# Kernel tuning notes

Measured on AMD Instinct MI355X. Metric: run time of the kernel, lower is better.

## Reference

```python
import jax, jax.numpy as jnp
import numpy as np

N = 100000
E = 1200000
D_IN = 64
D_OUT = 64
NUM_TYPES = 2


def setup_inputs() -> dict:
    key = jax.random.key(0)
    k1, k2, k3, k4, k5 = jax.random.split(key, 5)
    x = jax.random.normal(k1, (N, D_IN), dtype=jnp.float32)
    W = jax.random.normal(k2, (NUM_TYPES, D_IN, D_OUT), dtype=jnp.float32) / np.sqrt(D_IN)
    b = jax.random.normal(k3, (NUM_TYPES, D_OUT), dtype=jnp.float32) * 0.01
    edge_index = jax.random.randint(k4, (2, E), 0, N, dtype=jnp.int64)
    edge_attr = jax.random.randint(k5, (E,), 0, NUM_TYPES, dtype=jnp.int64)
    return {"x": x, "W": W, "b": b, "edge_index": edge_index, "edge_attr": edge_attr}


def reference(x, W, b, edge_index, edge_attr):
    # PyG flow source_to_target: x_j = x[src], aggregate at dst
    src, dst = edge_index[0], edge_index[1]
    x_j = x[src]                                   # [E, D_IN] gather
    # HeteroLinear with 2 types: compute both small GEMMs, select per edge
    m0 = x_j @ W[0] + b[0]                          # [E, D_OUT]
    m1 = x_j @ W[1] + b[1]                          # [E, D_OUT]
    msg = jnp.where((edge_attr == 0)[:, None], m0, m1)
    # scatter-max aggregation; PyG fills nodes with no incoming edges with 0
    agg = jax.ops.segment_max(msg, dst, num_segments=x.shape[0])
    out = jnp.where(jnp.isneginf(agg), 0.0, agg)
    return out
```

## Files before the change

kernel.cpp:

```cpp
#include <hip/hip_runtime.h>
#include <math.h>

static constexpr int D = 64;
static constexpr int SCAN_BLOCKS = 256;
static constexpr int NB_CHUNK = 96;
static constexpr int BIN_SHIFT = 6;
static constexpr int MAXBINS = 2048;

typedef __bf16 bf16x8 __attribute__((ext_vector_type(8)));
typedef float f32x4 __attribute__((ext_vector_type(4)));


__device__ __forceinline__ unsigned short f2bf(float f) {
  unsigned u = __float_as_uint(f);
  return (unsigned short)((u + 0x7fffu + ((u >> 16) & 1u)) >> 16);
}
__device__ __forceinline__ float bf2f(unsigned short h) {
  return __uint_as_float((unsigned)h << 16);
}

__device__ __forceinline__ void lds_max_f32(float* p, float v) {
  if (v >= 0.0f)
    atomicMax(reinterpret_cast<int*>(p), __float_as_int(v));
  else
    atomicMin(reinterpret_cast<unsigned int*>(p), __float_as_uint(v));
}

__device__ __forceinline__ void atomic_max_float(float* p, float v, float cur) {
  if (!(v > cur)) return;
  if (v >= 0.0f)
    atomicMax(reinterpret_cast<int*>(p), __float_as_int(v));
  else
    atomicMin(reinterpret_cast<unsigned int*>(p), __float_as_uint(v));
}

__global__ void k_init_neginf(float4* __restrict__ out, int n4) {
  int i = blockIdx.x * blockDim.x + threadIdx.x;
  if (i < n4) {
    float4 v;
    v.x = v.y = v.z = v.w = -INFINITY;
    out[i] = v;
  }
}

__global__ __launch_bounds__(256) void k_gemm(
    const float* __restrict__ x, const float* __restrict__ W,
    const float* __restrict__ b, unsigned short* __restrict__ yb, int nN) {
  const int lane = threadIdx.x & 63;
  const int wid = (blockIdx.x << 2) + (threadIdx.x >> 6);
  const int nWaves = gridDim.x << 2;
  const int kgrp = (lane >> 4) << 3;
  const int nsub = lane & 15;

  bf16x8 Bf[8][2];
  float bias[8];
#pragma unroll
  for (int nt = 0; nt < 8; ++nt) {
    const int t = nt >> 2;
    const int n = ((nt & 3) << 4) + nsub;
#pragma unroll
    for (int ks = 0; ks < 2; ++ks) {
      bf16x8 f;
#pragma unroll
      for (int e = 0; e < 8; ++e) {
        const int k = (ks << 5) + kgrp + e;
        f[e] = (__bf16)W[t * 4096 + k * 64 + n];
      }
      Bf[nt][ks] = f;
    }
    bias[nt] = b[t * 64 + n];
  }

  const int nChunks = (nN + 15) >> 4;
  for (int c = wid; c < nChunks; c += nWaves) {
    const int base = c << 4;
    const int arow = min(base + nsub, nN - 1);
    const float4 xa0 = *reinterpret_cast<const float4*>(x + (size_t)arow * 64 + kgrp);
    const float4 xa1 = *reinterpret_cast<const float4*>(x + (size_t)arow * 64 + kgrp + 4);
    const float4 xb0 = *reinterpret_cast<const float4*>(x + (size_t)arow * 64 + 32 + kgrp);
    const float4 xb1 = *reinterpret_cast<const float4*>(x + (size_t)arow * 64 + 36 + kgrp);
    bf16x8 a0, a1;
    a0[0] = (__bf16)xa0.x; a0[1] = (__bf16)xa0.y; a0[2] = (__bf16)xa0.z; a0[3] = (__bf16)xa0.w;
    a0[4] = (__bf16)xa1.x; a0[5] = (__bf16)xa1.y; a0[6] = (__bf16)xa1.z; a0[7] = (__bf16)xa1.w;
    a1[0] = (__bf16)xb0.x; a1[1] = (__bf16)xb0.y; a1[2] = (__bf16)xb0.z; a1[3] = (__bf16)xb0.w;
    a1[4] = (__bf16)xb1.x; a1[5] = (__bf16)xb1.y; a1[6] = (__bf16)xb1.z; a1[7] = (__bf16)xb1.w;
#pragma unroll
    for (int nt = 0; nt < 8; ++nt) {
      f32x4 acc = {bias[nt], bias[nt], bias[nt], bias[nt]};
      acc = __builtin_amdgcn_mfma_f32_16x16x32_bf16(a0, Bf[nt][0], acc, 0, 0, 0);
      acc = __builtin_amdgcn_mfma_f32_16x16x32_bf16(a1, Bf[nt][1], acc, 0, 0, 0);
      const int t = nt >> 2;
      const int o = ((nt & 3) << 4) + nsub;
      const int rbase = base + ((lane >> 4) << 2);
#pragma unroll
      for (int r = 0; r < 4; ++r) {
        const int node = rbase + r;
        if (node < nN) yb[((size_t)t * nN + node) * 64 + o] = f2bf(acc[r]);
      }
    }
  }
}


__global__ __launch_bounds__(1024) void k_lochist(const int* __restrict__ dst,
                                                  int* __restrict__ countsT,
                                                  int nE, int nBins, int chunk) {
  __shared__ int lh[MAXBINS];
  const int t = threadIdx.x;
  for (int i = t; i < nBins; i += 1024) lh[i] = 0;
  __syncthreads();
  const int beg = blockIdx.x * chunk;
  const int end = min(beg + chunk, nE);
  for (int i = beg + t; i < end; i += 1024) atomicAdd(&lh[dst[i] >> BIN_SHIFT], 1);
  __syncthreads();
  for (int i = t; i < nBins; i += 1024)
    countsT[(size_t)i * gridDim.x + blockIdx.x] = lh[i];
}

__global__ __launch_bounds__(256) void k_scan_partial(
    const int* __restrict__ counts, int* __restrict__ blockSums, int nN) {
  __shared__ int red[256];
  const int t = threadIdx.x;
  const int seg = (nN + gridDim.x - 1) / gridDim.x;
  const int beg = blockIdx.x * seg;
  const int end = min(beg + seg, nN);
  int s = 0;
  for (int i = beg + t; i < end; i += 256) s += counts[i];
  red[t] = s;
  __syncthreads();
  for (int d = 128; d > 0; d >>= 1) {
    if (t < d) red[t] += red[t + d];
    __syncthreads();
  }
  if (t == 0) blockSums[blockIdx.x] = red[0];
}

__global__ __launch_bounds__(256) void k_scan_block(
    int* __restrict__ blockSums, int* __restrict__ offs, int nN, int nBlocks) {
  __shared__ int sh[256];
  const int t = threadIdx.x;
  const int v = (t < nBlocks) ? blockSums[t] : 0;
  sh[t] = v;
  __syncthreads();
  for (int d = 1; d < 256; d <<= 1) {
    const int o = (t >= d) ? sh[t - d] : 0;
    __syncthreads();
    sh[t] += o;
    __syncthreads();
  }
  if (t < nBlocks) blockSums[t] = sh[t] - v;
  if (t == 255) offs[nN] = sh[255];
}

__global__ __launch_bounds__(256) void k_scan_write(
    const int* __restrict__ counts, const int* __restrict__ blockSums,
    int* __restrict__ offs, int nN) {
  __shared__ int sh[256];
  const int t = threadIdx.x;
  const int seg = (nN + gridDim.x - 1) / gridDim.x;
  const int beg = blockIdx.x * seg;
  const int end = min(beg + seg, nN);
  int carry = blockSums[blockIdx.x];
  for (int base = beg; base < end; base += 256) {
    const int i = base + t;
    const int v = (i < end) ? counts[i] : 0;
    sh[t] = v;
    __syncthreads();
    for (int d = 1; d < 256; d <<= 1) {
      const int o = (t >= d) ? sh[t - d] : 0;
      __syncthreads();
      sh[t] += o;
      __syncthreads();
    }
    if (i < end) offs[i] = carry + sh[t] - v;
    carry += sh[255];
    __syncthreads();
  }
}

__global__ __launch_bounds__(1024) void k_cscatter(
    const int* __restrict__ src, const int* __restrict__ dst,
    const int* __restrict__ ea, const int* __restrict__ offs,
    unsigned* __restrict__ rec, int nE, int nBins, int chunk) {
  __shared__ int cur[MAXBINS];
  const int t = threadIdx.x;
  for (int i = t; i < nBins; i += 1024)
    cur[i] = offs[(size_t)i * gridDim.x + blockIdx.x];
  __syncthreads();
  const int beg = blockIdx.x * chunk;
  const int end = min(beg + chunk, nE);
  for (int i = beg + t; i < end; i += 1024) {
    const int d = dst[i];
    const int pos = atomicAdd(&cur[d >> BIN_SHIFT], 1);
    rec[pos] = (unsigned)src[i] | ((unsigned)ea[i] << 20) |
               ((unsigned)(d & ((1 << BIN_SHIFT) - 1)) << 21);
  }
}

__global__ __launch_bounds__(256) void k_reduce_bin(
    const int* __restrict__ offs, const unsigned* __restrict__ rec,
    const unsigned short* __restrict__ yb, float* __restrict__ out, int nN) {
  __shared__ float acc[64 * 64];
  const int t = threadIdx.x;
#pragma unroll
  for (int i = 0; i < 16; ++i) acc[t + i * 256] = -INFINITY;
  __syncthreads();

  const int bin = blockIdx.x;
  const int beg = offs[bin * NB_CHUNK];
  const int cnt = offs[(bin + 1) * NB_CHUNK] - beg;
  const int w = t >> 6;
  const unsigned lane = t & 63;
  const unsigned nNu = (unsigned)nN;
  const int myBeg = beg + ((cnt * w) >> 2);
  const int myEnd = beg + ((cnt * (w + 1)) >> 2);

  int j = myBeg;
  for (; j + 7 < myEnd; j += 8) {
    unsigned r[8];
    float v[8];
#pragma unroll
    for (int q = 0; q < 8; ++q) r[q] = rec[j + q];
#pragma unroll
    for (int q = 0; q < 8; ++q)
      v[q] = bf2f(yb[((((r[q] >> 20) & 1u) * nNu + (r[q] & 0xFFFFFu)) << 6) + lane]);
#pragma unroll
    for (int q = 0; q < 8; ++q)
      lds_max_f32(&acc[(((r[q] >> 21) & 63u) << 6) + lane], v[q]);
  }
  for (; j + 3 < myEnd; j += 4) {
    unsigned r[4];
    float v[4];
#pragma unroll
    for (int q = 0; q < 4; ++q) r[q] = rec[j + q];
#pragma unroll
    for (int q = 0; q < 4; ++q)
      v[q] = bf2f(yb[((((r[q] >> 20) & 1u) * nNu + (r[q] & 0xFFFFFu)) << 6) + lane]);
#pragma unroll
    for (int q = 0; q < 4; ++q)
      lds_max_f32(&acc[(((r[q] >> 21) & 63u) << 6) + lane], v[q]);
  }
  for (; j < myEnd; ++j) {
    const unsigned r0 = rec[j];
    const float v0 = bf2f(yb[((((r0 >> 20) & 1u) * nNu + (r0 & 0xFFFFFu)) << 6) + lane]);
    lds_max_f32(&acc[(((r0 >> 21) & 63u) << 6) + lane], v0);
  }
  __syncthreads();

  const int nodeBase = bin << 6;
  for (int f = t; f < 64 * 16; f += 256) {
    const int node = nodeBase + (f >> 4);
    if (node < nN) {
      float4 v = *reinterpret_cast<const float4*>(&acc[f * 4]);
      if (v.x == -INFINITY) v.x = 0.0f;
      if (v.y == -INFINITY) v.y = 0.0f;
      if (v.z == -INFINITY) v.z = 0.0f;
      if (v.w == -INFINITY) v.w = 0.0f;
      *reinterpret_cast<float4*>(&out[(size_t)node * 64 + (f & 15) * 4]) = v;
    }
  }
}


__global__ void k_fixup(float4* __restrict__ out, int n4) {
  int i = blockIdx.x * blockDim.x + threadIdx.x;
  if (i < n4) {
    float4 v = out[i];
    if (v.x == -INFINITY) v.x = 0.0f;
    if (v.y == -INFINITY) v.y = 0.0f;
    if (v.z == -INFINITY) v.z = 0.0f;
    if (v.w == -INFINITY) v.w = 0.0f;
    out[i] = v;
  }
}

__global__ __launch_bounds__(256) void k_edge_direct(
    const float* __restrict__ x, const float* __restrict__ W,
    const float* __restrict__ b, const int* __restrict__ ei,
    const int* __restrict__ ea, float* __restrict__ out, int nEdges) {
  __shared__ float Wl[2 * D * D];
  __shared__ float bl[2 * D];
  for (int i = threadIdx.x; i < 2 * D * D; i += 256) Wl[i] = W[i];
  for (int i = threadIdx.x; i < 2 * D; i += 256) bl[i] = b[i];
  __syncthreads();
  const int wave = threadIdx.x >> 6;
  const int lane = threadIdx.x & 63;
  for (int e = blockIdx.x * 4 + wave; e < nEdges; e += gridDim.x * 4) {
    const int src = ei[e];
    const int dst = ei[nEdges + e];
    const int t = ea[e];
    const float xk = x[(size_t)src * D + lane];
    float acc = bl[t * D + lane];
    const float* Wt = &Wl[t * D * D];
#pragma unroll
    for (int k = 0; k < D; ++k)
      acc = fmaf(__shfl(xk, k, 64), Wt[k * D + lane], acc);
    float* p = out + (size_t)dst * D + lane;
    const float cur = *p;
    atomic_max_float(p, acc, cur);
  }
}


extern "C" void kernel_launch(void* const* d_in, const int* in_sizes, int n_in,
                              void* d_out, int out_size, void* d_ws, size_t ws_size,
                              hipStream_t stream) {
  const float* x = (const float*)d_in[0];
  const float* W = (const float*)d_in[1];
  const float* b = (const float*)d_in[2];
  const int* ei = (const int*)d_in[3];
  const int* ea = (const int*)d_in[4];
  float* out = (float*)d_out;

  const int nNodes = in_sizes[0] / D;
  const int nEdges = in_sizes[4];
  const int n4out = (nNodes * D) / 4;
  const int nBins = (nNodes + (1 << BIN_SHIFT) - 1) >> BIN_SHIFT;
  const int nScan = nBins * NB_CHUNK;
  const int chunk = (nEdges + NB_CHUNK - 1) / NB_CHUNK;

  auto rup = [](size_t v) { return (v + 255) & ~(size_t)255; };
  const size_t ybB = (size_t)2 * nNodes * D * sizeof(unsigned short);
  const size_t offYb = 0;
  const size_t offCT = rup(offYb + ybB);
  const size_t offOffs = rup(offCT + (size_t)nScan * sizeof(int));
  const size_t offBS = rup(offOffs + (size_t)(nScan + 1) * sizeof(int));
  const size_t offRec = rup(offBS + (size_t)SCAN_BLOCKS * sizeof(int));
  const size_t need = offRec + (size_t)nEdges * sizeof(unsigned);

  if (ws_size >= need && nNodes < (1 << 20) && nBins <= MAXBINS) {
    char* ws = (char*)d_ws;
    unsigned short* yb = (unsigned short*)(ws + offYb);
    int* countsT = (int*)(ws + offCT);
    int* offs = (int*)(ws + offOffs);
    int* blockSums = (int*)(ws + offBS);
    unsigned* rec = (unsigned*)(ws + offRec);

    const int* srcRow = ei;
    const int* dstRow = ei + nEdges;

    k_lochist<<<NB_CHUNK, 1024, 0, stream>>>(dstRow, countsT, nEdges, nBins, chunk);
    k_scan_partial<<<SCAN_BLOCKS, 256, 0, stream>>>(countsT, blockSums, nScan);
    k_scan_block<<<1, 256, 0, stream>>>(blockSums, offs, nScan, SCAN_BLOCKS);
    k_scan_write<<<SCAN_BLOCKS, 256, 0, stream>>>(countsT, blockSums, offs, nScan);
    k_cscatter<<<NB_CHUNK, 1024, 0, stream>>>(srcRow, dstRow, ea, offs, rec,
                                              nEdges, nBins, chunk);
    k_gemm<<<512, 256, 0, stream>>>(x, W, b, yb, nNodes);
    k_reduce_bin<<<nBins, 256, 0, stream>>>(offs, rec, yb, out, nNodes);
  } else {
    k_init_neginf<<<(n4out + 255) / 256, 256, 0, stream>>>((float4*)out, n4out);
    k_edge_direct<<<4096, 256, 0, stream>>>(x, W, b, ei, ea, out, nEdges);
    k_fixup<<<(n4out + 255) / 256, 256, 0, stream>>>((float4*)out, n4out);
  }
}
```

Before: 190.6 us.

## Use order-preserving bf16 encoding for unsigned LDS max, fuse scan, widen reduce blocks

The GEMM now stores bf16 outputs in a monotone unsigned encoding, so the bin reducer can use a single unsigned atomicMax in LDS instead of a sign-dependent max/min branch. Zero serves as the empty sentinel and is decoded back to 0.0 at write-out. The separate single-block scan-of-block-sums kernel is folded into k_scan_write, which removes one launch at the cost of every block redundantly scanning the 256 partial sums. The reducer also moves to 512 threads with 8 waves per bin to add memory-level parallelism, and its 4-wide tail loop is dropped.

```diff
diff --git a/kernel.cpp b/kernel.cpp
--- a/kernel.cpp
+++ b/kernel.cpp
@@ -15,15 +15,17 @@
   unsigned u = __float_as_uint(f);
   return (unsigned short)((u + 0x7fffu + ((u >> 16) & 1u)) >> 16);
 }
-__device__ __forceinline__ float bf2f(unsigned short h) {
-  return __uint_as_float((unsigned)h << 16);
-}
-
-__device__ __forceinline__ void lds_max_f32(float* p, float v) {
-  if (v >= 0.0f)
-    atomicMax(reinterpret_cast<int*>(p), __float_as_int(v));
-  else
-    atomicMin(reinterpret_cast<unsigned int*>(p), __float_as_uint(v));
+
+__device__ __forceinline__ unsigned short bf_enc(unsigned short u) {
+  const unsigned short s = (unsigned short)(-(int)(u >> 15));
+  return (unsigned short)(u ^ (s | 0x8000u));
+}
+__device__ __forceinline__ float bf_dec_to_f32(unsigned enc32) {
+  if (enc32 == 0u) return 0.0f;
+  unsigned short enc = (unsigned short)(enc32 >> 16);
+  unsigned short u = (enc & 0x8000u) ? (unsigned short)(enc ^ 0x8000u)
+                                     : (unsigned short)(~enc);
+  return __uint_as_float((unsigned)u << 16);
 }
 
 __device__ __forceinline__ void atomic_max_float(float* p, float v, float cur) {
@@ -95,7 +97,8 @@
 #pragma unroll
       for (int r = 0; r < 4; ++r) {
         const int node = rbase + r;
-        if (node < nN) yb[((size_t)t * nN + node) * 64 + o] = f2bf(acc[r]);
+        if (node < nN)
+          yb[((size_t)t * nN + node) * 64 + o] = bf_enc(f2bf(acc[r]));
       }
     }
   }
@@ -135,32 +138,26 @@
   if (t == 0) blockSums[blockIdx.x] = red[0];
 }
 
-__global__ __launch_bounds__(256) void k_scan_block(
-    int* __restrict__ blockSums, int* __restrict__ offs, int nN, int nBlocks) {
-  __shared__ int sh[256];
-  const int t = threadIdx.x;
-  const int v = (t < nBlocks) ? blockSums[t] : 0;
-  sh[t] = v;
-  __syncthreads();
-  for (int d = 1; d < 256; d <<= 1) {
-    const int o = (t >= d) ? sh[t - d] : 0;
-    __syncthreads();
-    sh[t] += o;
-    __syncthreads();
-  }
-  if (t < nBlocks) blockSums[t] = sh[t] - v;
-  if (t == 255) offs[nN] = sh[255];
-}
-
 __global__ __launch_bounds__(256) void k_scan_write(
     const int* __restrict__ counts, const int* __restrict__ blockSums,
     int* __restrict__ offs, int nN) {
+  __shared__ int bs[256];
   __shared__ int sh[256];
   const int t = threadIdx.x;
+  bs[t] = blockSums[t];
+  __syncthreads();
+  for (int d = 1; d < 256; d <<= 1) {
+    const int o = (t >= d) ? bs[t - d] : 0;
+    __syncthreads();
+    bs[t] += o;
+    __syncthreads();
+  }
+  const int bid = blockIdx.x;
+  int carry = (bid > 0) ? bs[bid - 1] : 0;
+  const int total = bs[255];
   const int seg = (nN + gridDim.x - 1) / gridDim.x;
-  const int beg = blockIdx.x * seg;
+  const int beg = bid * seg;
   const int end = min(beg + seg, nN);
-  int carry = blockSums[blockIdx.x];
   for (int base = beg; base < end; base += 256) {
     const int i = base + t;
     const int v = (i < end) ? counts[i] : 0;
@@ -176,6 +173,7 @@
     carry += sh[255];
     __syncthreads();
   }
+  if (bid == gridDim.x - 1 && t == 0) offs[nN] = total;
 }
 
 __global__ __launch_bounds__(1024) void k_cscatter(
@@ -197,13 +195,13 @@
   }
 }
 
-__global__ __launch_bounds__(256) void k_reduce_bin(
+__global__ __launch_bounds__(512) void k_reduce_bin(
     const int* __restrict__ offs, const unsigned* __restrict__ rec,
     const unsigned short* __restrict__ yb, float* __restrict__ out, int nN) {
-  __shared__ float acc[64 * 64];
-  const int t = threadIdx.x;
-#pragma unroll
-  for (int i = 0; i < 16; ++i) acc[t + i * 256] = -INFINITY;
+  __shared__ unsigned acc[64 * 64];
+  const int t = threadIdx.x;
+#pragma unroll
+  for (int i = 0; i < 8; ++i) acc[t + i * 512] = 0u;
   __syncthreads();
 
   const int bin = blockIdx.x;
@@ -212,50 +210,39 @@
   const int w = t >> 6;
   const unsigned lane = t & 63;
   const unsigned nNu = (unsigned)nN;
-  const int myBeg = beg + ((cnt * w) >> 2);
-  const int myEnd = beg + ((cnt * (w + 1)) >> 2);
+  const int myBeg = beg + ((cnt * w) >> 3);
+  const int myEnd = beg + ((cnt * (w + 1)) >> 3);
 
   int j = myBeg;
   for (; j + 7 < myEnd; j += 8) {
     unsigned r[8];
-    float v[8];
+    unsigned v[8];
 #pragma unroll
     for (int q = 0; q < 8; ++q) r[q] = rec[j + q];
 #pragma unroll
     for (int q = 0; q < 8; ++q)
-      v[q] = bf2f(yb[((((r[q] >> 20) & 1u) * nNu + (r[q] & 0xFFFFFu)) << 6) + lane]);
+      v[q] = (unsigned)yb[((((r[q] >> 20) & 1u) * nNu + (r[q] & 0xFFFFFu)) << 6) + lane] << 16;
 #pragma unroll
     for (int q = 0; q < 8; ++q)
-      lds_max_f32(&acc[(((r[q] >> 21) & 63u) << 6) + lane], v[q]);
-  }
-  for (; j + 3 < myEnd; j += 4) {
-    unsigned r[4];
-    float v[4];
-#pragma unroll
-    for (int q = 0; q < 4; ++q) r[q] = rec[j + q];
-#pragma unroll
-    for (int q = 0; q < 4; ++q)
-      v[q] = bf2f(yb[((((r[q] >> 20) & 1u) * nNu + (r[q] & 0xFFFFFu)) << 6) + lane]);
-#pragma unroll
-    for (int q = 0; q < 4; ++q)
-      lds_max_f32(&acc[(((r[q] >> 21) & 63u) << 6) + lane], v[q]);
+      atomicMax(&acc[(((r[q] >> 21) & 63u) << 6) + lane], v[q]);
   }
   for (; j < myEnd; ++j) {
     const unsigned r0 = rec[j];
-    const float v0 = bf2f(yb[((((r0 >> 20) & 1u) * nNu + (r0 & 0xFFFFFu)) << 6) + lane]);
-    lds_max_f32(&acc[(((r0 >> 21) & 63u) << 6) + lane], v0);
+    const unsigned v0 =
+        (unsigned)yb[((((r0 >> 20) & 1u) * nNu + (r0 & 0xFFFFFu)) << 6) + lane] << 16;
+    atomicMax(&acc[(((r0 >> 21) & 63u) << 6) + lane], v0);
   }
   __syncthreads();
 
   const int nodeBase = bin << 6;
-  for (int f = t; f < 64 * 16; f += 256) {
+  for (int f = t; f < 64 * 16; f += 512) {
     const int node = nodeBase + (f >> 4);
     if (node < nN) {
-      float4 v = *reinterpret_cast<const float4*>(&acc[f * 4]);
-      if (v.x == -INFINITY) v.x = 0.0f;
-      if (v.y == -INFINITY) v.y = 0.0f;
-      if (v.z == -INFINITY) v.z = 0.0f;
-      if (v.w == -INFINITY) v.w = 0.0f;
+      float4 v;
+      v.x = bf_dec_to_f32(acc[f * 4 + 0]);
+      v.y = bf_dec_to_f32(acc[f * 4 + 1]);
+      v.z = bf_dec_to_f32(acc[f * 4 + 2]);
+      v.w = bf_dec_to_f32(acc[f * 4 + 3]);
       *reinterpret_cast<float4*>(&out[(size_t)node * 64 + (f & 15) * 4]) = v;
     }
   }
@@ -341,12 +328,11 @@
 
     k_lochist<<<NB_CHUNK, 1024, 0, stream>>>(dstRow, countsT, nEdges, nBins, chunk);
     k_scan_partial<<<SCAN_BLOCKS, 256, 0, stream>>>(countsT, blockSums, nScan);
-    k_scan_block<<<1, 256, 0, stream>>>(blockSums, offs, nScan, SCAN_BLOCKS);
     k_scan_write<<<SCAN_BLOCKS, 256, 0, stream>>>(countsT, blockSums, offs, nScan);
     k_cscatter<<<NB_CHUNK, 1024, 0, stream>>>(srcRow, dstRow, ea, offs, rec,
                                               nEdges, nBins, chunk);
     k_gemm<<<512, 256, 0, stream>>>(x, W, b, yb, nNodes);
-    k_reduce_bin<<<nBins, 256, 0, stream>>>(offs, rec, yb, out, nNodes);
+    k_reduce_bin<<<nBins, 512, 0, stream>>>(offs, rec, yb, out, nNodes);
   } else {
     k_init_neginf<<<(n4out + 255) / 256, 256, 0, stream>>>((float4*)out, n4out);
     k_edge_direct<<<4096, 256, 0, stream>>>(x, W, b, ei, ea, out, nEdges);
```

After: 167.1 us. 1.14x faster.
